# Performance work log

Measured on AMD Instinct MI355X. Metric: run time of the kernel, lower is better.

## Reference

```python
import jax, jax.numpy as jnp
import numpy as np

B, CIN, H, W = 8, 64, 56, 56
COUT, K, HEADS, PAD = 64, 7, 8, 3


def hswish(x):
    return x * jnp.clip(x + 3.0, 0.0, 6.0) / 6.0


def grouped_1x1(x, w):
    # x: (B, Cin, H, W); w: (G, Cout_g, Cin_g)  -> (B, Cout, H, W)
    b, cin, h, wd = x.shape
    g = w.shape[0]
    xg = x.reshape(b, g, cin // g, h, wd)
    y = jnp.einsum('bgihw,goi->bgohw', xg, w)
    return y.reshape(b, g * w.shape[1], h, wd)


def unfold2d(x, k, h_out, w_out):
    # x: (B, C, Hp, Wp) -> (B, C, h_out, w_out, k, k), stride 1
    cols = [x[:, :, i:i + h_out, j:j + w_out] for i in range(k) for j in range(k)]
    s = jnp.stack(cols, axis=-1)  # (B,C,h,w,k*k) in (kh,kw) row-major order
    return s.reshape(*s.shape[:-1], k, k)


def setup_inputs() -> dict:
    key = jax.random.key(0)
    k1, k2, k3, k4, k5, k6 = jax.random.split(key, 6)
    cin_g, cout_g = CIN // HEADS, COUT // HEADS
    fan_out = cout_g  # 1x1 kernel, kaiming fan_out per group
    std = float(np.sqrt(2.0 / fan_out))
    return {
        'x': jax.random.normal(k1, (B, CIN, H, W), dtype=jnp.float32),
        'wq': jax.random.normal(k2, (HEADS, cout_g, cin_g), dtype=jnp.float32) * std,
        'wk': jax.random.normal(k3, (HEADS, cout_g, cin_g), dtype=jnp.float32) * std,
        'wv': jax.random.normal(k4, (HEADS, cout_g, cin_g), dtype=jnp.float32) * std,
        'rel_h': jax.random.normal(k5, (COUT // 2, 1, 1, K, 1), dtype=jnp.float32),
        'rel_w': jax.random.normal(k6, (COUT // 2, 1, 1, 1, K), dtype=jnp.float32),
    }


def reference(x, wq, wk, wv, rel_h, rel_w):
    b, _, h, w = x.shape
    heads = wq.shape[0]
    d = COUT // heads
    padded = jnp.pad(x, ((0, 0), (0, 0), (PAD, PAD), (PAD, PAD)))
    q = grouped_1x1(x, wq)                       # (B, Cout, H, W)
    k_full = grouped_1x1(padded, wk)             # (B, Cout, Hp, Wp)
    v_full = hswish(grouped_1x1(padded, wv))
    kp = unfold2d(k_full, K, h, w)               # (B, Cout, H, W, K, K)
    vp = unfold2d(v_full, K, h, w)
    kh, kw_ = kp[:, :COUT // 2], kp[:, COUT // 2:]
    kp = jnp.concatenate((kh + rel_h, kw_ + rel_w), axis=1)
    kp = kp.reshape(b, heads, d, h, w, K * K)
    vp = vp.reshape(b, heads, d, h, w, K * K)
    qh = q.reshape(b, heads, d, h, w, 1)
    # NOTE: faithful to original bug: sqrt(heads // out_channels) == 0.0
    scale = float(np.sqrt(heads // COUT))
    logits = (qh * kp).sum(axis=2, keepdims=True) * scale  # (B,heads,1,H,W,K*K)
    attn = jax.nn.softmax(logits, axis=-1)
    out = (attn * vp).sum(axis=-1)               # (B, heads, d, H, W)
    return out.reshape(b, heads * d, h, w)
```

## Files before the change

### kernel.cpp

```cpp
#include <hip/hip_runtime.h>


namespace {
constexpr int Bn = 8, CINn = 64, Hn = 56, Wn = 56;
constexpr int HEADSn = 8, CGn = 8;
constexpr int PADn = 3;
constexpr int TH = 4;
constexpr int NTILES = Hn / TH;
constexpr int PH = TH + 6;
constexpr int PW = Wn + 6;
constexpr int NP = PH * PW;
constexpr int NHS = PH * Wn;
constexpr int NOUT = TH * Wn;
constexpr int THREADS = 256;
}

__global__ __launch_bounds__(THREADS) void saconv_fused(
    const float* __restrict__ x, const float* __restrict__ wv,
    float* __restrict__ out)
{
    __shared__ float wvs[64];
    __shared__ float vt[NP * 8];
    __shared__ float hs[NHS * 8];

    const int bid  = blockIdx.x;
    const int tile = bid % NTILES;
    const int g    = (bid / NTILES) % HEADSn;
    const int b    = bid / (NTILES * HEADSn);
    const int h0   = tile * TH;
    const int tid  = threadIdx.x;

    if (tid < 64) wvs[tid] = wv[g * 64 + tid];
    __syncthreads();

    const float* __restrict__ xg =
        x + (size_t)(b * CINn + g * CGn) * (Hn * Wn);

    for (int p = tid; p < NP; p += THREADS) {
        const int py = p / PW;
        const int px = p - py * PW;
        const int y  = h0 + py - PADn;
        const int xx = px - PADn;
        float v[8];
        if (y >= 0 && y < Hn && xx >= 0 && xx < Wn) {
            float in[8];
            #pragma unroll
            for (int i = 0; i < 8; ++i)
                in[i] = xg[i * (Hn * Wn) + y * Wn + xx];
            #pragma unroll
            for (int o = 0; o < 8; ++o) {
                float a = 0.0f;
                #pragma unroll
                for (int i = 0; i < 8; ++i)
                    a = fmaf(wvs[o * 8 + i], in[i], a);
                float t = fminf(fmaxf(a + 3.0f, 0.0f), 6.0f);
                v[o] = a * t * (1.0f / 6.0f);
            }
        } else {
            #pragma unroll
            for (int o = 0; o < 8; ++o) v[o] = 0.0f;
        }
        #pragma unroll
        for (int o = 0; o < 8; ++o) vt[p * 8 + o] = v[o];
    }
    __syncthreads();

    for (int p = tid; p < NHS; p += THREADS) {
        const int y  = p / Wn;
        const int xx = p - y * Wn;
        float s[8] = {0, 0, 0, 0, 0, 0, 0, 0};
        #pragma unroll
        for (int j = 0; j < 7; ++j) {
            const float* src = &vt[(y * PW + xx + j) * 8];
            #pragma unroll
            for (int o = 0; o < 8; ++o) s[o] += src[o];
        }
        #pragma unroll
        for (int o = 0; o < 8; ++o) hs[p * 8 + o] = s[o];
    }
    __syncthreads();

    if (tid < NOUT) {
        const int ty = tid / Wn;
        const int tx = tid - ty * Wn;
        float s[8] = {0, 0, 0, 0, 0, 0, 0, 0};
        #pragma unroll
        for (int i = 0; i < 7; ++i) {
            const float* src = &hs[((ty + i) * Wn + tx) * 8];
            #pragma unroll
            for (int o = 0; o < 8; ++o) s[o] += src[o];
        }
        const float inv = 1.0f / 49.0f;
        float* og = out + ((size_t)(b * CINn + g * CGn) * Hn + (h0 + ty)) * Wn + tx;
        #pragma unroll
        for (int o = 0; o < 8; ++o)
            og[o * (Hn * Wn)] = s[o] * inv;
    }
}

extern "C" void kernel_launch(void* const* d_in, const int* in_sizes, int n_in,
                              void* d_out, int out_size, void* d_ws, size_t ws_size,
                              hipStream_t stream) {
    const float* x  = (const float*)d_in[0];
    const float* wv = (const float*)d_in[3];
    float* out = (float*)d_out;

    dim3 grid(Bn * HEADSn * NTILES);
    saconv_fused<<<grid, THREADS, 0, stream>>>(x, wv, out);
}
```

Baseline: 12.84 us.

## Restructure box-filter stages with float4 smem layout and two-output sliding sums

Stores the hswish(v) tile in shared memory as two float4 channel-half planes with a padded, skewed row index to reduce bank conflicts. The vertical and horizontal 7-tap box sums now each compute two adjacent outputs per thread by reusing a running sum, cutting redundant shared loads and adds. Output is written as float2 pairs. Fewer threads are active in the reduction stages, which may lower parallelism within the block.

```diff
diff --git a/kernel.cpp b/kernel.cpp
--- a/kernel.cpp
+++ b/kernel.cpp
@@ -3,25 +3,32 @@
 
 namespace {
 constexpr int Bn = 8, CINn = 64, Hn = 56, Wn = 56;
-constexpr int HEADSn = 8, CGn = 8;
+constexpr int HEADSn = 8;
 constexpr int PADn = 3;
 constexpr int TH = 4;
 constexpr int NTILES = Hn / TH;
 constexpr int PH = TH + 6;
 constexpr int PW = Wn + 6;
-constexpr int NP = PH * PW;
-constexpr int NHS = PH * Wn;
-constexpr int NOUT = TH * Wn;
+constexpr int RS = 80;
 constexpr int THREADS = 256;
+constexpr int NRUNS = Wn / 2;
 }
 
-__global__ __launch_bounds__(THREADS) void saconv_fused(
+__device__ __forceinline__ int sx(int x) { return x + (x >> 2); }
+__device__ __forceinline__ float4 f4add(float4 a, float4 b) {
+    return make_float4(a.x + b.x, a.y + b.y, a.z + b.z, a.w + b.w);
+}
+__device__ __forceinline__ float4 f4sub(float4 a, float4 b) {
+    return make_float4(a.x - b.x, a.y - b.y, a.z - b.z, a.w - b.w);
+}
+
+__global__ __launch_bounds__(THREADS) void saconv_r2(
     const float* __restrict__ x, const float* __restrict__ wv,
     float* __restrict__ out)
 {
-    __shared__ float wvs[64];
-    __shared__ float vt[NP * 8];
-    __shared__ float hs[NHS * 8];
+    __shared__ float  wvs[64];
+    __shared__ float4 vt[2 * PH * RS];
+    __shared__ float4 vs[2 * TH * RS];
 
     const int bid  = blockIdx.x;
     const int tile = bid % NTILES;
@@ -33,68 +40,79 @@
     if (tid < 64) wvs[tid] = wv[g * 64 + tid];
     __syncthreads();
 
-    const float* __restrict__ xg =
-        x + (size_t)(b * CINn + g * CGn) * (Hn * Wn);
+    const float* __restrict__ xg = x + (size_t)(b * CINn + g * 8) * (Hn * Wn);
 
-    for (int p = tid; p < NP; p += THREADS) {
+    for (int p = tid; p < PH * PW; p += THREADS) {
         const int py = p / PW;
         const int px = p - py * PW;
         const int y  = h0 + py - PADn;
         const int xx = px - PADn;
-        float v[8];
-        if (y >= 0 && y < Hn && xx >= 0 && xx < Wn) {
+        float4 v0 = make_float4(0.f, 0.f, 0.f, 0.f);
+        float4 v1 = v0;
+        if ((unsigned)y < (unsigned)Hn && (unsigned)xx < (unsigned)Wn) {
             float in[8];
             #pragma unroll
             for (int i = 0; i < 8; ++i)
                 in[i] = xg[i * (Hn * Wn) + y * Wn + xx];
+            float a[8];
             #pragma unroll
             for (int o = 0; o < 8; ++o) {
-                float a = 0.0f;
+                float s = 0.f;
                 #pragma unroll
                 for (int i = 0; i < 8; ++i)
-                    a = fmaf(wvs[o * 8 + i], in[i], a);
-                float t = fminf(fmaxf(a + 3.0f, 0.0f), 6.0f);
-                v[o] = a * t * (1.0f / 6.0f);
+                    s = fmaf(wvs[o * 8 + i], in[i], s);
+                float t = fminf(fmaxf(s + 3.f, 0.f), 6.f);
+                a[o] = s * t * (1.f / 6.f);
             }
-        } else {
-            #pragma unroll
-            for (int o = 0; o < 8; ++o) v[o] = 0.0f;
+            v0 = make_float4(a[0], a[1], a[2], a[3]);
+            v1 = make_float4(a[4], a[5], a[6], a[7]);
         }
-        #pragma unroll
-        for (int o = 0; o < 8; ++o) vt[p * 8 + o] = v[o];
+        vt[(0 * PH + py) * RS + sx(px)] = v0;
+        vt[(1 * PH + py) * RS + sx(px)] = v1;
     }
     __syncthreads();
 
-    for (int p = tid; p < NHS; p += THREADS) {
-        const int y  = p / Wn;
-        const int xx = p - y * Wn;
-        float s[8] = {0, 0, 0, 0, 0, 0, 0, 0};
+    if (tid < 2 * PW * 2) {
+        const int g4 = tid & 1;
+        const int r  = tid >> 1;
+        const int xx = r % PW;
+        const int yh = r / PW;
+        const int y0 = 2 * yh;
+        float4 rv[8];
         #pragma unroll
-        for (int j = 0; j < 7; ++j) {
-            const float* src = &vt[(y * PW + xx + j) * 8];
-            #pragma unroll
-            for (int o = 0; o < 8; ++o) s[o] += src[o];
-        }
+        for (int j = 0; j < 8; ++j)
+            rv[j] = vt[(g4 * PH + y0 + j) * RS + sx(xx)];
+        float4 s = rv[0];
         #pragma unroll
-        for (int o = 0; o < 8; ++o) hs[p * 8 + o] = s[o];
+        for (int j = 1; j < 7; ++j) s = f4add(s, rv[j]);
+        vs[(g4 * TH + y0) * RS + sx(xx)] = s;
+        s = f4add(s, f4sub(rv[7], rv[0]));
+        vs[(g4 * TH + y0 + 1) * RS + sx(xx)] = s;
     }
     __syncthreads();
 
-    if (tid < NOUT) {
-        const int ty = tid / Wn;
-        const int tx = tid - ty * Wn;
-        float s[8] = {0, 0, 0, 0, 0, 0, 0, 0};
+    if (tid < TH * NRUNS * 2) {
+        const int g4  = tid & 1;
+        const int r   = tid >> 1;
+        const int run = r % NRUNS;
+        const int y   = r / NRUNS;
+        const int x0  = run * 2;
+        float4 rv[8];
         #pragma unroll
-        for (int i = 0; i < 7; ++i) {
-            const float* src = &hs[((ty + i) * Wn + tx) * 8];
-            #pragma unroll
-            for (int o = 0; o < 8; ++o) s[o] += src[o];
-        }
-        const float inv = 1.0f / 49.0f;
-        float* og = out + ((size_t)(b * CINn + g * CGn) * Hn + (h0 + ty)) * Wn + tx;
+        for (int j = 0; j < 8; ++j)
+            rv[j] = vs[(g4 * TH + y) * RS + sx(x0 + j)];
+        float4 s0 = rv[0];
         #pragma unroll
-        for (int o = 0; o < 8; ++o)
-            og[o * (Hn * Wn)] = s[o] * inv;
+        for (int j = 1; j < 7; ++j) s0 = f4add(s0, rv[j]);
+        float4 s1 = f4add(s0, f4sub(rv[7], rv[0]));
+        const float inv = 1.f / 49.f;
+        float* ob = out + ((size_t)(b * CINn + g * 8 + g4 * 4) * Hn + (h0 + y)) * Wn + x0;
+        const int plane = Hn * Wn;
+        float2 st;
+        st.x = s0.x * inv; st.y = s1.x * inv; *(float2*)(ob + 0 * plane) = st;
+        st.x = s0.y * inv; st.y = s1.y * inv; *(float2*)(ob + 1 * plane) = st;
+        st.x = s0.z * inv; st.y = s1.z * inv; *(float2*)(ob + 2 * plane) = st;
+        st.x = s0.w * inv; st.y = s1.w * inv; *(float2*)(ob + 3 * plane) = st;
     }
 }
 
@@ -106,5 +124,5 @@
     float* out = (float*)d_out;
 
     dim3 grid(Bn * HEADSn * NTILES);
-    saconv_fused<<<grid, THREADS, 0, stream>>>(x, wv, out);
+    saconv_r2<<<grid, THREADS, 0, stream>>>(x, wv, out);
 }
```

Measured after the change: 11.75 us. -8.5%, faster.
